# Optimization experiments

Measured on AMD Instinct MI355X. Metric: run time of the kernel, lower is better.

The kernel has to match this reference:

```python
import jax, jax.numpy as jnp
import numpy as np

B, N, D_MODEL, LAP = 64, 64, 256, 16


def setup_inputs() -> dict:
    key = jax.random.key(0)
    ks = jax.random.split(key, 8)
    adj = jax.random.randint(ks[0], (B, N, N), 0, 2, dtype=jnp.int32)
    node_feats = jax.random.normal(ks[1], (B, N, D_MODEL), dtype=jnp.float32)
    eigvec = jax.random.normal(ks[2], (B, N, LAP), dtype=jnp.float32)
    W_lap = jax.random.normal(ks[3], (LAP, D_MODEL), dtype=jnp.float32) / np.sqrt(LAP)
    W_edge = jax.random.normal(ks[4], (1 + 2 * LAP, D_MODEL), dtype=jnp.float32) / np.sqrt(1 + 2 * LAP)
    b_edge = jax.random.normal(ks[5], (D_MODEL,), dtype=jnp.float32) * 0.02
    type_embed = jax.random.normal(ks[6], (2, D_MODEL), dtype=jnp.float32)
    graph_tok = jax.random.normal(ks[7], (1, 1, D_MODEL), dtype=jnp.float32)
    return {"adj": adj, "node_feats": node_feats, "eigvec": eigvec,
            "W_lap": W_lap, "W_edge": W_edge, "b_edge": b_edge,
            "type_embed": type_embed, "graph_tok": graph_tok}


def reference(adj, node_feats, eigvec, W_lap, W_edge, b_edge, type_embed, graph_tok):
    b, n, _ = adj.shape
    d = graph_tok.shape[-1]
    # node tokens: feats + LapPE projection
    node_tok = node_feats + jnp.einsum('bnl,ld->bnd', eigvec, W_lap)
    # upper-triangular candidate edges (fixed M = n(n-1)/2, jit-friendly)
    iu, ju = jnp.triu_indices(n, k=1)               # [M]
    valid = adj[:, iu, ju] > 0                       # [B, M]
    # stable compaction: valid edges first (matches torch per-graph extraction order)
    order = jnp.argsort(~valid, axis=1, stable=True) # [B, M]
    src = iu[order]                                  # [B, M]
    dst = ju[order]
    valid_sorted = jnp.take_along_axis(valid, order, axis=1)
    Pu = jnp.take_along_axis(eigvec, src[..., None], axis=1)  # [B, M, LAP]
    Pv = jnp.take_along_axis(eigvec, dst[..., None], axis=1)
    m = src.shape[1]
    edge_in = jnp.concatenate([jnp.ones((b, m, 1), eigvec.dtype), Pu, Pv], axis=-1)
    etok = jnp.einsum('bmf,fd->bmd', edge_in, W_edge) + b_edge + type_embed[1]
    etok = jnp.where(valid_sorted[..., None], etok, 0.0)      # zeros at padding
    pad_mask_edges = ~valid_sorted                             # True = padding
    gtok = jnp.broadcast_to(graph_tok, (b, 1, d))
    seq_embeds = jnp.concatenate([gtok, node_tok, etok], axis=1)  # [B, 1+n+M, d]
    pad_mask = jnp.concatenate([jnp.zeros((b, 1 + n), bool), pad_mask_edges], axis=1)
    return seq_embeds, pad_mask
```

## Files before the change

kernel.cpp:

```cpp
#include <hip/hip_runtime.h>

#define B_ 64
#define N_ 64
#define D_ 256
#define LAP_ 16
#define M_ 2016
#define TOK_ 2081

__device__ __forceinline__ void ij_from_m(int m, int& i, int& j) {
    float fm = (float)m;
    int gi = (int)((127.0f - sqrtf(127.0f * 127.0f - 8.0f * fm)) * 0.5f);
    if (gi < 0) gi = 0;
    if (gi > 62) gi = 62;
    while (gi > 0 && (127 * gi - gi * gi) / 2 > m) gi--;
    while (gi < 62 && (127 * (gi + 1) - (gi + 1) * (gi + 1)) / 2 <= m) gi++;
    i = gi;
    j = gi + 1 + (m - (127 * gi - gi * gi) / 2);
}

__global__ __launch_bounds__(256, 2) void fused_kernel(
    const int*   __restrict__ adj,
    const float* __restrict__ node_feats,
    const float* __restrict__ eigvec,
    const float* __restrict__ W_lap,
    const float* __restrict__ W_edge,
    const float* __restrict__ b_edge,
    const float* __restrict__ type_embed,
    const float* __restrict__ graph_tok,
    float*       __restrict__ out)
{
    __shared__ float sEig[N_ * LAP_];
    __shared__ float sU[N_ * 64];
    __shared__ float sV[N_ * 64];
    __shared__ int   sDest[M_];
    __shared__ unsigned long long sWords[32];
    __shared__ int sPref[32];
    __shared__ int sTotal;

    const int b    = blockIdx.x;
    const int cg   = blockIdx.y;
    const int t    = threadIdx.x;
    const int wave = t >> 6, lane = t & 63;
    const int c    = cg * 64 + lane;

    ((float4*)sEig)[t] = ((const float4*)(eigvec + (size_t)b * N_ * LAP_))[t];

    int ival[8];
    int av[8];
#pragma unroll
    for (int k = 0; k < 8; k++) {
        int m = k * 256 + t;
        int i = 0, j = 0;
        if (m < M_) {
            ij_from_m(m, i, j);
            av[k] = adj[b * (N_ * N_) + i * N_ + j];
        } else av[k] = 0;
        ival[k] = i | (j << 6);
    }

    float base = W_edge[c] + b_edge[c] + type_embed[D_ + c];
    float w1c[LAP_], w2c[LAP_], wlc[LAP_];
#pragma unroll
    for (int l = 0; l < LAP_; l++) {
        w1c[l] = W_edge[(1 + l) * D_ + c];
        w2c[l] = W_edge[(1 + LAP_ + l) * D_ + c];
        wlc[l] = W_lap[l * D_ + c];
    }

#pragma unroll
    for (int k = 0; k < 8; k++) {
        int valid = (k * 256 + t < M_) && (av[k] > 0);
        unsigned long long blt = __ballot(valid);
        if (lane == 0) sWords[k * 4 + wave] = blt;
        ival[k] |= valid << 12;
    }
    __syncthreads();

    if (t < 32) {
        unsigned long long word = sWords[t];
        int cnt = __popcll(word);
        int inc = cnt;
#pragma unroll
        for (int off = 1; off < 32; off <<= 1) {
            int v = __shfl_up(inc, off);
            if (lane >= off) inc += v;
        }
        sPref[t] = inc - cnt;
        if (t == 31) sTotal = inc;
    }

#pragma unroll 2
    for (int n16 = 0; n16 < 16; n16++) {
        int n = wave * 16 + n16;
        const float* e = sEig + n * LAP_;
        float accU = 0.0f, accV = 0.0f;
#pragma unroll
        for (int l = 0; l < LAP_; l++) {
            float el = e[l];
            accU += el * w1c[l];
            accV += el * w2c[l];
        }
        sU[n * 64 + lane] = accU;
        sV[n * 64 + lane] = accV;
    }
    __syncthreads();

    const int total = sTotal;
    float* maskb = out + (size_t)B_ * TOK_ * D_ + (size_t)b * TOK_;
#pragma unroll
    for (int k = 0; k < 8; k++) {
        int m = k * 256 + t;
        if (m < M_) {
            int w = k * 4 + wave;
            unsigned long long word = sWords[w];
            int rank = sPref[w] + __popcll(word & ((1ull << lane) - 1ull));
            int valid = (ival[k] >> 12) & 1;
            int p = valid ? rank : total + (m - rank);
            sDest[m] = (ival[k] & 0xFFF) | (valid << 12) | (p << 13);
            if (cg == 0) maskb[1 + N_ + p] = valid ? 0.0f : 1.0f;
        }
    }

    float* outB = out + (size_t)b * TOK_ * D_;
#pragma unroll 2
    for (int n16 = 0; n16 < 16; n16++) {
        int n = wave * 16 + n16;
        float a = node_feats[((size_t)b * N_ + n) * D_ + c];
        const float* e = sEig + n * LAP_;
#pragma unroll
        for (int l = 0; l < LAP_; l++) a += e[l] * wlc[l];
        __builtin_nontemporal_store(a, outB + (size_t)(1 + n) * D_ + c);
    }
    if (wave == 0) outB[c] = graph_tok[c];
    if (cg == 0 && t < 1 + N_) maskb[t] = 0.0f;
    __syncthreads();

    float* outE = outB + (size_t)(1 + N_) * D_;
#pragma unroll 4
    for (int q = 0; q < M_ / 4; q++) {
        int m = wave * (M_ / 4) + q;
        int info = sDest[m];
        int p = info >> 13;
        float val = 0.0f;
        if (info & (1 << 12)) {
            int si = info & 63, di = (info >> 6) & 63;
            val = base + sU[si * 64 + lane] + sV[di * 64 + lane];
        }
        __builtin_nontemporal_store(val, outE + (size_t)p * D_ + c);
    }
}

extern "C" void kernel_launch(void* const* d_in, const int* in_sizes, int n_in,
                              void* d_out, int out_size, void* d_ws, size_t ws_size,
                              hipStream_t stream) {
    const int*   adj        = (const int*)d_in[0];
    const float* node_feats = (const float*)d_in[1];
    const float* eigvec     = (const float*)d_in[2];
    const float* W_lap      = (const float*)d_in[3];
    const float* W_edge     = (const float*)d_in[4];
    const float* b_edge     = (const float*)d_in[5];
    const float* type_embed = (const float*)d_in[6];
    const float* graph_tok  = (const float*)d_in[7];
    float* out = (float*)d_out;

    fused_kernel<<<dim3(B_, 4), dim3(256), 0, stream>>>(
        adj, node_feats, eigvec, W_lap, W_edge, b_edge, type_embed, graph_tok, out);
}
```

Baseline: 187.4 us.

## Split edges across blocks and emit full-width float4 edge rows

```diff
diff --git a/kernel.cpp b/kernel.cpp
--- a/kernel.cpp
+++ b/kernel.cpp
@@ -6,6 +6,10 @@
 #define LAP_ 16
 #define M_ 2016
 #define TOK_ 2081
+#define MPB_ 504
+#define MPW_ 126
+
+typedef float v4f __attribute__((ext_vector_type(4)));
 
 __device__ __forceinline__ void ij_from_m(int m, int& i, int& j) {
     float fm = (float)m;
@@ -18,7 +22,7 @@
     j = gi + 1 + (m - (127 * gi - gi * gi) / 2);
 }
 
-__global__ __launch_bounds__(256, 2) void fused_kernel(
+__global__ __launch_bounds__(256, 1) void fused_kernel(
     const int*   __restrict__ adj,
     const float* __restrict__ node_feats,
     const float* __restrict__ eigvec,
@@ -30,55 +34,47 @@
     float*       __restrict__ out)
 {
     __shared__ float sEig[N_ * LAP_];
-    __shared__ float sU[N_ * 64];
-    __shared__ float sV[N_ * 64];
-    __shared__ int   sDest[M_];
+    __shared__ float sU[N_ * D_];
+    __shared__ float sV[N_ * D_];
     __shared__ unsigned long long sWords[32];
     __shared__ int sPref[32];
+    __shared__ int sDest[MPB_];
     __shared__ int sTotal;
 
     const int b    = blockIdx.x;
     const int cg   = blockIdx.y;
     const int t    = threadIdx.x;
     const int wave = t >> 6, lane = t & 63;
-    const int c    = cg * 64 + lane;
 
     ((float4*)sEig)[t] = ((const float4*)(eigvec + (size_t)b * N_ * LAP_))[t];
-
-    int ival[8];
-    int av[8];
 #pragma unroll
     for (int k = 0; k < 8; k++) {
         int m = k * 256 + t;
-        int i = 0, j = 0;
+        int valid = 0;
         if (m < M_) {
+            int i, j;
             ij_from_m(m, i, j);
-            av[k] = adj[b * (N_ * N_) + i * N_ + j];
-        } else av[k] = 0;
-        ival[k] = i | (j << 6);
+            valid = (adj[b * (N_ * N_) + i * N_ + j] > 0) ? 1 : 0;
+        }
+        unsigned long long blt = __ballot(valid);
+        if (lane == 0) sWords[k * 4 + wave] = blt;
     }
 
-    float base = W_edge[c] + b_edge[c] + type_embed[D_ + c];
     float w1c[LAP_], w2c[LAP_], wlc[LAP_];
 #pragma unroll
     for (int l = 0; l < LAP_; l++) {
-        w1c[l] = W_edge[(1 + l) * D_ + c];
-        w2c[l] = W_edge[(1 + LAP_ + l) * D_ + c];
-        wlc[l] = W_lap[l * D_ + c];
+        w1c[l] = W_edge[(1 + l) * D_ + t];
+        w2c[l] = W_edge[(1 + LAP_ + l) * D_ + t];
+        wlc[l] = W_lap[l * D_ + t];
     }
+    v4f base4 = *((const v4f*)W_edge + lane);
+    base4 += *((const v4f*)b_edge + lane);
+    base4 += *((const v4f*)(type_embed + D_) + lane);
 
-#pragma unroll
-    for (int k = 0; k < 8; k++) {
-        int valid = (k * 256 + t < M_) && (av[k] > 0);
-        unsigned long long blt = __ballot(valid);
-        if (lane == 0) sWords[k * 4 + wave] = blt;
-        ival[k] |= valid << 12;
-    }
     __syncthreads();
 
     if (t < 32) {
-        unsigned long long word = sWords[t];
-        int cnt = __popcll(word);
+        int cnt = __popcll(sWords[t]);
         int inc = cnt;
 #pragma unroll
         for (int off = 1; off < 32; off <<= 1) {
@@ -89,64 +85,68 @@
         if (t == 31) sTotal = inc;
     }
 
-#pragma unroll 2
-    for (int n16 = 0; n16 < 16; n16++) {
-        int n = wave * 16 + n16;
-        const float* e = sEig + n * LAP_;
-        float accU = 0.0f, accV = 0.0f;
-#pragma unroll
-        for (int l = 0; l < LAP_; l++) {
-            float el = e[l];
-            accU += el * w1c[l];
-            accV += el * w2c[l];
-        }
-        sU[n * 64 + lane] = accU;
-        sV[n * 64 + lane] = accV;
+#pragma unroll 4
+    for (int n = 0; n < N_; n++) {
+        const v4f* e4 = (const v4f*)(sEig + n * LAP_);
+        v4f e0 = e4[0], e1 = e4[1], e2 = e4[2], e3 = e4[3];
+        float aU, aV;
+        aU  = e0.x * w1c[0]  + e0.y * w1c[1]  + e0.z * w1c[2]  + e0.w * w1c[3];
+        aU += e1.x * w1c[4]  + e1.y * w1c[5]  + e1.z * w1c[6]  + e1.w * w1c[7];
+        aU += e2.x * w1c[8]  + e2.y * w1c[9]  + e2.z * w1c[10] + e2.w * w1c[11];
+        aU += e3.x * w1c[12] + e3.y * w1c[13] + e3.z * w1c[14] + e3.w * w1c[15];
+        aV  = e0.x * w2c[0]  + e0.y * w2c[1]  + e0.z * w2c[2]  + e0.w * w2c[3];
+        aV += e1.x * w2c[4]  + e1.y * w2c[5]  + e1.z * w2c[6]  + e1.w * w2c[7];
+        aV += e2.x * w2c[8]  + e2.y * w2c[9]  + e2.z * w2c[10] + e2.w * w2c[11];
+        aV += e3.x * w2c[12] + e3.y * w2c[13] + e3.z * w2c[14] + e3.w * w2c[15];
+        sU[n * D_ + t] = aU;
+        sV[n * D_ + t] = aV;
     }
     __syncthreads();
 
     const int total = sTotal;
     float* maskb = out + (size_t)B_ * TOK_ * D_ + (size_t)b * TOK_;
-#pragma unroll
-    for (int k = 0; k < 8; k++) {
-        int m = k * 256 + t;
-        if (m < M_) {
-            int w = k * 4 + wave;
-            unsigned long long word = sWords[w];
-            int rank = sPref[w] + __popcll(word & ((1ull << lane) - 1ull));
-            int valid = (ival[k] >> 12) & 1;
-            int p = valid ? rank : total + (m - rank);
-            sDest[m] = (ival[k] & 0xFFF) | (valid << 12) | (p << 13);
-            if (cg == 0) maskb[1 + N_ + p] = valid ? 0.0f : 1.0f;
-        }
+    for (int idx = t; idx < MPB_; idx += 256) {
+        int m = cg * MPB_ + idx;
+        int w = m >> 6, r = m & 63;
+        unsigned long long word = sWords[w];
+        int rank = sPref[w] + __popcll(word & ((1ull << r) - 1ull));
+        int valid = (int)((word >> r) & 1ull);
+        int p = valid ? rank : total + (m - rank);
+        int i, j;
+        ij_from_m(m, i, j);
+        sDest[idx] = i | (j << 6) | (valid << 12) | (p << 13);
+        maskb[1 + N_ + p] = valid ? 0.0f : 1.0f;
     }
 
     float* outB = out + (size_t)b * TOK_ * D_;
-#pragma unroll 2
-    for (int n16 = 0; n16 < 16; n16++) {
-        int n = wave * 16 + n16;
-        float a = node_feats[((size_t)b * N_ + n) * D_ + c];
+#pragma unroll 4
+    for (int k = 0; k < 16; k++) {
+        int n = cg * 16 + k;
+        float a = node_feats[((size_t)b * N_ + n) * D_ + t];
         const float* e = sEig + n * LAP_;
 #pragma unroll
         for (int l = 0; l < LAP_; l++) a += e[l] * wlc[l];
-        __builtin_nontemporal_store(a, outB + (size_t)(1 + n) * D_ + c);
+        __builtin_nontemporal_store(a, outB + (size_t)(1 + n) * D_ + t);
     }
-    if (wave == 0) outB[c] = graph_tok[c];
-    if (cg == 0 && t < 1 + N_) maskb[t] = 0.0f;
+    if (cg == 0) {
+        outB[t] = graph_tok[t];
+        if (t < 1 + N_) maskb[t] = 0.0f;
+    }
     __syncthreads();
 
     float* outE = outB + (size_t)(1 + N_) * D_;
-#pragma unroll 4
-    for (int q = 0; q < M_ / 4; q++) {
-        int m = wave * (M_ / 4) + q;
-        int info = sDest[m];
+#pragma unroll 2
+    for (int q = 0; q < MPW_; q++) {
+        int info = sDest[wave * MPW_ + q];
         int p = info >> 13;
-        float val = 0.0f;
+        v4f val = {0.0f, 0.0f, 0.0f, 0.0f};
         if (info & (1 << 12)) {
             int si = info & 63, di = (info >> 6) & 63;
-            val = base + sU[si * 64 + lane] + sV[di * 64 + lane];
+            v4f u = ((const v4f*)(sU + si * D_))[lane];
+            v4f v = ((const v4f*)(sV + di * D_))[lane];
+            val = base4 + u + v;
         }
-        __builtin_nontemporal_store(val, outE + (size_t)p * D_ + c);
+        __builtin_nontemporal_store(val, (v4f*)(outE + (size_t)p * D_) + lane);
     }
 }
 
```

Measured after the change: 179.5 us. -4.2%, faster.
